# Kernel tuning notes

Measured on AMD Instinct MI355X. Metric: run time of the kernel, lower is better.

Reference implementation:

```python
import jax, jax.numpy as jnp
import numpy as np

SCALES = (16, 32, 64, 128)
P = 8
D = 1024
H = 16
DEPTH = 8
MLP = 4096
NCLS = 1000
PB = [(s // P) ** 2 for s in SCALES]            # [4, 16, 64, 256]
BLOCKS = [PB[0] + 1] + PB[1:]                    # [5, 16, 64, 256]
L = sum(BLOCKS)                                  # 341
PATCH_L = sum(PB)                                # 340
PD = P * P * 3                                   # 192
HD = D // H
EPS = 1e-6

# scale id per token (start token belongs to scale 0)
_SID = np.concatenate([np.full(n, k, dtype=np.int32) for k, n in enumerate(BLOCKS)])
# additive block-causal mask: token in scale q may attend to scales <= q
_ALLOW = _SID[None, :] <= _SID[:, None]
MASK = jnp.where(jnp.asarray(_ALLOW), 0.0, -1e30).astype(jnp.float32)  # [L, L]
SID = jnp.asarray(_SID)


def _ln(x):
    m = jnp.mean(x, axis=-1, keepdims=True)
    v = jnp.var(x, axis=-1, keepdims=True)
    return (x - m) / jnp.sqrt(v + EPS)


def _l2n(t):
    n = jnp.sqrt(jnp.sum(t * t, axis=-1, keepdims=True))
    return t / jnp.maximum(n, 1e-12)


def setup_inputs() -> dict:
    key = jax.random.key(0)
    ks = jax.random.split(key, 16)
    s = 0.02
    inp = {
        "patches": jax.random.normal(ks[0], (8, PATCH_L, PD), jnp.float32),
        "labels": jax.random.randint(ks[1], (8,), 0, NCLS),
        "W_patch": s * jax.random.normal(ks[2], (PD, D), jnp.float32),
        "b_patch": jnp.zeros((D,), jnp.float32),
        "pos": s * jax.random.normal(ks[3], (1, L, D), jnp.float32),
        "scale_emb": s * jax.random.normal(ks[4], (len(SCALES), D), jnp.float32),
        "class_emb": s * jax.random.normal(ks[5], (NCLS + 1, D), jnp.float32),
        "ada_W": s * jax.random.normal(ks[6], (DEPTH, D, 6 * D), jnp.float32),
        "ada_b": jnp.zeros((DEPTH, 6 * D), jnp.float32),
        "qkv_W": s * jax.random.normal(ks[7], (DEPTH, D, 3 * D), jnp.float32),
        "qkv_b": jnp.zeros((DEPTH, 3 * D), jnp.float32),
        "q_scale": jnp.zeros((DEPTH, 1, 1, H, 1), jnp.float32),  # log-scale per head
        "proj_W": s * jax.random.normal(ks[8], (DEPTH, D, D), jnp.float32),
        "proj_b": jnp.zeros((DEPTH, D), jnp.float32),
        "fc1_W": s * jax.random.normal(ks[9], (DEPTH, D, MLP), jnp.float32),
        "fc1_b": jnp.zeros((DEPTH, MLP), jnp.float32),
        "fc2_W": s * jax.random.normal(ks[10], (DEPTH, MLP, D), jnp.float32),
        "fc2_b": jnp.zeros((DEPTH, D), jnp.float32),
        "head_ada_W": s * jax.random.normal(ks[11], (D, 2 * D), jnp.float32),
        "head_ada_b": jnp.zeros((2 * D,), jnp.float32),
        "head_W": s * jax.random.normal(ks[12], (D, PD), jnp.float32),
        "head_b": jnp.zeros((PD,), jnp.float32),
    }
    return inp


def reference(patches, labels, W_patch, b_patch, pos, scale_emb, class_emb,
              ada_W, ada_b, qkv_W, qkv_b, q_scale, proj_W, proj_b,
              fc1_W, fc1_b, fc2_W, fc2_b, head_ada_W, head_ada_b, head_W, head_b):
    B = patches.shape[0]
    cond = class_emb[labels]                              # [B, D]
    tok = patches @ W_patch + b_patch                     # [B, PATCH_L, D]
    x = jnp.concatenate([cond[:, None, :], tok], axis=1)  # [B, L, D]
    x = x + pos + scale_emb[SID]

    for i in range(DEPTH):
        ada = jax.nn.silu(cond) @ ada_W[i] + ada_b[i]     # [B, 6D]
        g1, g2, s1, s2, sh1, sh2 = [a[:, None, :] for a in jnp.split(ada, 6, axis=-1)]
        # attention branch
        h = _ln(x) * (s1 + 1.0) + sh1
        qkv = (h @ qkv_W[i] + qkv_b[i]).reshape(B, L, 3, H, HD)
        q, k, v = qkv[:, :, 0], qkv[:, :, 1], qkv[:, :, 2]  # [B, L, H, HD]
        q = _l2n(q) * jnp.exp(q_scale[i])                  # attn_l2_norm
        k = _l2n(k)
        scores = jnp.einsum("bqhd,bkhd->bhqk", q, k) + MASK
        attn = jax.nn.softmax(scores, axis=-1)
        o = jnp.einsum("bhqk,bkhd->bqhd", attn, v).reshape(B, L, D)
        x = x + g1 * (o @ proj_W[i] + proj_b[i])
        # mlp branch
        h2 = _ln(x) * (s2 + 1.0) + sh2
        m = jax.nn.gelu(h2 @ fc1_W[i] + fc1_b[i]) @ fc2_W[i] + fc2_b[i]
        x = x + g2 * m

    ada = jax.nn.silu(cond) @ head_ada_W + head_ada_b     # [B, 2D]
    sc, sh = [a[:, None, :] for a in jnp.split(ada, 2, axis=-1)]
    x = _ln(x) * (sc + 1.0) + sh
    return x @ head_W + head_b                            # [B, L, PD]
```

## Files before the change

kernel.cpp:

```cpp
#include <hip/hip_runtime.h>

typedef unsigned short ushort_t;
typedef __bf16 bf16x8 __attribute__((ext_vector_type(8)));
typedef float f32x4 __attribute__((ext_vector_type(4)));

#define DEV __device__ __forceinline__

DEV ushort_t f2bf(float x) {
  union { float f; unsigned u; } v; v.f = x;
  unsigned r = v.u + 0x7FFFu + ((v.u >> 16) & 1u);
  return (ushort_t)(r >> 16);
}
DEV float bf2f(ushort_t h) {
  union { unsigned u; float f; } v; v.u = (unsigned)h << 16;
  return v.f;
}
DEV int sid_of(int l) { return l < 5 ? 0 : (l < 21 ? 1 : (l < 85 ? 2 : 3)); }
DEV float fast_tanh(float u) { return 1.0f - 2.0f / (__expf(2.0f * u) + 1.0f); }
DEV float gelu_f(float x) {
  float u = 0.7978845608028654f * (x + 0.044715f * x * x * x);
  return 0.5f * x * (1.0f + fast_tanh(u));
}
DEV float silu_f(float x) { return x / (1.0f + __expf(-x)); }
DEV f32x4 mfma16(bf16x8 a, bf16x8 b, f32x4 c) {
  return __builtin_amdgcn_mfma_f32_16x16x32_bf16(a, b, c, 0, 0, 0);
}

DEV void gload16(const void* src, void* dst) {
  __builtin_amdgcn_global_load_lds(
      (const __attribute__((address_space(1))) void*)(uintptr_t)src,
      (__attribute__((address_space(3))) void*)(uintptr_t)dst, 16, 0, 0);
}

__global__ __launch_bounds__(256) void k_cond_x0(
    const int* __restrict__ labels, const float* __restrict__ class_emb,
    const float* __restrict__ pos, const float* __restrict__ semb,
    float* __restrict__ cond, float* __restrict__ x) {
  int b = blockIdx.x, t = threadIdx.x;
  int lab = labels[b];
  float4 cv = *(const float4*)&class_emb[(size_t)lab * 1024 + t * 4];
  *(float4*)&cond[(size_t)b * 1024 + t * 4] = cv;
  float4 pv = *(const float4*)&pos[t * 4];
  float4 sv = *(const float4*)&semb[t * 4];
  float4 xv;
  xv.x = cv.x + pv.x + sv.x; xv.y = cv.y + pv.y + sv.y;
  xv.z = cv.z + pv.z + sv.z; xv.w = cv.w + pv.w + sv.w;
  *(float4*)&x[(size_t)b * 341 * 1024 + t * 4] = xv;
}

__global__ __launch_bounds__(256) void k_convert(const float* __restrict__ src,
                                                 ushort_t* __restrict__ dst, int n4) {
  int i = blockIdx.x * 256 + threadIdx.x;
  if (i < n4) {
    float4 v = *(const float4*)&src[(size_t)i * 4];
    uint2 pk;
    pk.x = (unsigned)f2bf(v.x) | ((unsigned)f2bf(v.y) << 16);
    pk.y = (unsigned)f2bf(v.z) | ((unsigned)f2bf(v.w) << 16);
    *(uint2*)&dst[(size_t)i * 4] = pk;
  }
}

__global__ __launch_bounds__(256) void k_transpose(const float* __restrict__ src,
                                                   ushort_t* __restrict__ dst, int K, int N) {
  __shared__ ushort_t tile[32][33];
  int z = blockIdx.z;
  src += (size_t)z * K * N;
  dst += (size_t)z * K * N;
  int k0 = blockIdx.y * 32, n0 = blockIdx.x * 32;
  int t = threadIdx.x;
  int r = t >> 3, c = (t & 7) * 4;
  float4 v = *(const float4*)&src[(size_t)(k0 + r) * N + n0 + c];
  tile[r][c] = f2bf(v.x); tile[r][c + 1] = f2bf(v.y);
  tile[r][c + 2] = f2bf(v.z); tile[r][c + 3] = f2bf(v.w);
  __syncthreads();
  ushort_t o0 = tile[c][r], o1 = tile[c + 1][r], o2 = tile[c + 2][r], o3 = tile[c + 3][r];
  uint2 pk;
  pk.x = (unsigned)o0 | ((unsigned)o1 << 16);
  pk.y = (unsigned)o2 | ((unsigned)o3 << 16);
  *(uint2*)&dst[(size_t)(n0 + r) * K + k0 + c] = pk;
}

__global__ __launch_bounds__(256) void k_ada(const float* __restrict__ cond,
    const float* __restrict__ ada_W, const float* __restrict__ ada_b,
    const float* __restrict__ hada_W, const float* __restrict__ hada_b,
    float* __restrict__ ada_out, float* __restrict__ hada_out) {
  int gy = blockIdx.y;
  bool head = (gy == 8);
  int Nw = head ? 2048 : 6144;
  int n0 = blockIdx.x * 64;
  if (n0 >= Nw) return;
  __shared__ float sc[8 * 1024];
  __shared__ float red[4][64][8];
  int t = threadIdx.x;
  for (int i = t; i < 2048; i += 256) {
    float4 cv = *(const float4*)&cond[(size_t)i * 4];
    float* d = &sc[i * 4];
    d[0] = silu_f(cv.x); d[1] = silu_f(cv.y); d[2] = silu_f(cv.z); d[3] = silu_f(cv.w);
  }
  __syncthreads();
  const float* W = head ? hada_W : ada_W + (size_t)gy * 1024 * 6144;
  const float* bs = head ? hada_b : ada_b + (size_t)gy * 6144;
  float* op = head ? hada_out : ada_out + (size_t)gy * 8 * 6144;
  int col = n0 + (t & 63), kq = t >> 6;
  float acc[8] = {0.f, 0.f, 0.f, 0.f, 0.f, 0.f, 0.f, 0.f};
  for (int k = kq * 256; k < kq * 256 + 256; ++k) {
    float wv = W[(size_t)k * Nw + col];
#pragma unroll
    for (int b2 = 0; b2 < 8; ++b2) acc[b2] += wv * sc[b2 * 1024 + k];
  }
#pragma unroll
  for (int b2 = 0; b2 < 8; ++b2) red[kq][t & 63][b2] = acc[b2];
  __syncthreads();
  if (t < 64) {
    int colc = n0 + t;
    float bias = bs[colc];
#pragma unroll
    for (int b2 = 0; b2 < 8; ++b2) {
      float v = red[0][t][b2] + red[1][t][b2] + red[2][t][b2] + red[3][t][b2] + bias;
      op[(size_t)b2 * Nw + colc] = v;
    }
  }
}

__global__ __launch_bounds__(256) void k_ln(const float* __restrict__ x,
    ushort_t* __restrict__ hout, const float* __restrict__ ada,
    int stride, int soff, int shoff) {
  int row = blockIdx.x, t = threadIdx.x;
  int b = row / 341;
  const float* xr = x + (size_t)row * 1024;
  float4 xv = *(const float4*)&xr[t * 4];
  float s = xv.x + xv.y + xv.z + xv.w;
  float ss = xv.x * xv.x + xv.y * xv.y + xv.z * xv.z + xv.w * xv.w;
#pragma unroll
  for (int off = 1; off < 64; off <<= 1) { s += __shfl_xor(s, off); ss += __shfl_xor(ss, off); }
  __shared__ float red[8];
  int w = t >> 6, lane = t & 63;
  if (lane == 0) { red[w] = s; red[w + 4] = ss; }
  __syncthreads();
  s = red[0] + red[1] + red[2] + red[3];
  ss = red[4] + red[5] + red[6] + red[7];
  float mean = s * (1.f / 1024.f);
  float var = ss * (1.f / 1024.f) - mean * mean;
  float rstd = rsqrtf(var + 1e-6f);
  const float* ar = ada + (size_t)b * stride;
  float xe[4] = {xv.x, xv.y, xv.z, xv.w};
  ushort_t tmp[4];
#pragma unroll
  for (int j = 0; j < 4; ++j) {
    int n = t * 4 + j;
    float val = (xe[j] - mean) * rstd * (1.f + ar[soff + n]) + ar[shoff + n];
    tmp[j] = f2bf(val);
  }
  uint2 pk;
  pk.x = (unsigned)tmp[0] | ((unsigned)tmp[1] << 16);
  pk.y = (unsigned)tmp[2] | ((unsigned)tmp[3] << 16);
  *(uint2*)&hout[(size_t)row * 1024 + t * 4] = pk;
}

template <int EPI, int BM>
__global__ __launch_bounds__(256, 3) void k_gemm(
    const ushort_t* __restrict__ A, const ushort_t* __restrict__ Bt,
    const float* __restrict__ bias, float* __restrict__ fout,
    ushort_t* __restrict__ bfout, const float* __restrict__ aux,
    float* __restrict__ xres, const float* __restrict__ pos,
    const float* __restrict__ semb, int M, int N, int K, int KS) {
  constexpr int NI = (BM == 128) ? 4 : 2;
  constexpr int WNB = (BM == 128) ? 64 : 32;
  __shared__ ushort_t aT[2][BM * 32];
  __shared__ ushort_t bT[2][128 * 32];
  int tid = threadIdx.x;
  int lane = tid & 63, w = tid >> 6;
  int WR = (BM == 128) ? (w >> 1) : 0;
  int WC = (BM == 128) ? (w & 1) : w;

  int gx = gridDim.x;
  int nwg = gx * gridDim.y;
  int orig = blockIdx.y * gx + blockIdx.x;
  int q = nwg >> 3, r8 = nwg & 7;
  int xcd = orig & 7, idx = orig >> 3;
  int lin = (xcd < r8 ? xcd * (q + 1) : r8 * (q + 1) + (xcd - r8) * q) + idx;
  int bx = lin % gx, by = lin / gx;

  int m0 = by * BM, n0 = bx * 128;
  int kbase = blockIdx.z * KS;
  f32x4 acc[4][NI];
#pragma unroll
  for (int i = 0; i < 4; ++i)
#pragma unroll
    for (int j = 0; j < NI; ++j) acc[i][j] = (f32x4){0.f, 0.f, 0.f, 0.f};

  int lrow = lane & 15;
  int csw = (lrow >> 1) & 3;
  int coff = ((lane >> 4) ^ csw) * 8;

  int s_row0 = tid >> 2, s_u = tid & 3;
  int s_c = s_u ^ ((s_row0 >> 1) & 3);
  int aR0 = m0 + s_row0; if (aR0 > M - 1) aR0 = M - 1;
  int bR0 = n0 + s_row0; if (bR0 > N - 1) bR0 = N - 1;
  int aR1 = m0 + s_row0 + 64; if (aR1 > M - 1) aR1 = M - 1;
  int bR1 = n0 + s_row0 + 64; if (bR1 > N - 1) bR1 = N - 1;
  const ushort_t* aSrc0 = A + (size_t)aR0 * K + kbase + s_c * 8;
  const ushort_t* aSrc1 = A + (size_t)aR1 * K + kbase + s_c * 8;
  const ushort_t* bSrc0 = Bt + (size_t)bR0 * K + kbase + s_c * 8;
  const ushort_t* bSrc1 = Bt + (size_t)bR1 * K + kbase + s_c * 8;
  int slot0 = w * 512, slot1 = 2048 + w * 512;

  int nsteps = KS >> 5;
  auto STAGE = [&](int k0, int buf) {
    gload16(aSrc0 + k0, &aT[buf][slot0]);
    if constexpr (BM == 128) gload16(aSrc1 + k0, &aT[buf][slot1]);
    gload16(bSrc0 + k0, &bT[buf][slot0]);
    gload16(bSrc1 + k0, &bT[buf][slot1]);
  };

  STAGE(0, 0);
  int cur = 0;
  for (int s = 0; s < nsteps; ++s) {
    int kn = (s + 1 < nsteps) ? ((s + 1) << 5) : 0;
    STAGE(kn, cur ^ 1);
    if constexpr (BM == 128)
      asm volatile("s_waitcnt vmcnt(4)" ::: "memory");
    else
      asm volatile("s_waitcnt vmcnt(3)" ::: "memory");
    __builtin_amdgcn_sched_barrier(0);
    __builtin_amdgcn_s_barrier();
    __builtin_amdgcn_sched_barrier(0);
    bf16x8 af[4], bb[NI];
#pragma unroll
    for (int mi = 0; mi < 4; ++mi)
      af[mi] = *(const bf16x8*)&aT[cur][(WR * 64 + mi * 16 + lrow) * 32 + coff];
#pragma unroll
    for (int ni = 0; ni < NI; ++ni)
      bb[ni] = *(const bf16x8*)&bT[cur][(WC * WNB + ni * 16 + lrow) * 32 + coff];
#pragma unroll
    for (int mi = 0; mi < 4; ++mi)
#pragma unroll
      for (int ni = 0; ni < NI; ++ni)
        acc[mi][ni] = mfma16(af[mi], bb[ni], acc[mi][ni]);
    __builtin_amdgcn_sched_barrier(0);
    __builtin_amdgcn_s_barrier();
    __builtin_amdgcn_sched_barrier(0);
    cur ^= 1;
  }

  if constexpr (EPI == 6) {
    int nb = n0 + WC * 64;
    int gh = nb >> 6;
    float qse = (gh < 16) ? __expf(aux[gh]) : 1.0f;
    bool dn = gh < 32;
#pragma unroll
    for (int mi = 0; mi < 4; ++mi) {
#pragma unroll
      for (int r = 0; r < 4; ++r) {
        float vv[4]; float ss = 0.f;
#pragma unroll
        for (int ni = 0; ni < 4; ++ni) {
          vv[ni] = acc[mi][ni][r] + bias[nb + ni * 16 + lrow];
          ss += vv[ni] * vv[ni];
        }
        if (dn) {
          ss += __shfl_xor(ss, 1); ss += __shfl_xor(ss, 2);
          ss += __shfl_xor(ss, 4); ss += __shfl_xor(ss, 8);
          float rn = qse / fmaxf(sqrtf(ss), 1e-12f);
#pragma unroll
          for (int ni = 0; ni < 4; ++ni) vv[ni] *= rn;
        }
        int gm = m0 + WR * 64 + mi * 16 + (lane >> 4) * 4 + r;
        if (gm < M) {
#pragma unroll
          for (int ni = 0; ni < 4; ++ni)
            bfout[(size_t)gm * N + nb + ni * 16 + lrow] = f2bf(vv[ni]);
        }
      }
    }
  } else {
#pragma unroll
    for (int mi = 0; mi < 4; ++mi) {
#pragma unroll
      for (int ni = 0; ni < NI; ++ni) {
#pragma unroll
        for (int r = 0; r < 4; ++r) {
          int gm = m0 + WR * 64 + mi * 16 + (lane >> 4) * 4 + r;
          int gn = n0 + WC * WNB + ni * 16 + lrow;
          if (gm >= M || gn >= N) continue;
          if constexpr (EPI == 7) {
            fout[(size_t)blockIdx.z * M * N + (size_t)gm * N + gn] = acc[mi][ni][r];
          } else {
            float v = acc[mi][ni][r] + bias[gn];
            if constexpr (EPI == 1) {
              int b = gm / 341;
              xres[(size_t)gm * 1024 + gn] += aux[(size_t)b * 6144 + gn] * v;
            } else if constexpr (EPI == 2) {
              bfout[(size_t)gm * N + gn] = f2bf(gelu_f(v));
            } else if constexpr (EPI == 4) {
              int b = gm / 340, l = gm % 340 + 1;
              float val = v + pos[(size_t)l * 1024 + gn] + semb[(size_t)sid_of(l) * 1024 + gn];
              xres[((size_t)(b * 341 + l)) * 1024 + gn] = val;
            }
          }
        }
      }
    }
  }
}

template <int MODE>
__global__ __launch_bounds__(256) void k_comb(const float* __restrict__ p,
    const float* __restrict__ bias, const float* __restrict__ aux,
    float* __restrict__ xres, float* __restrict__ out, int N, int nsplit) {
  int row = blockIdx.x, t = threadIdx.x;
  size_t stride = (size_t)2728 * N;
  if constexpr (MODE == 0) {
    int c = t * 4;
    float4 s = *(const float4*)&p[(size_t)row * N + c];
    for (int sp = 1; sp < nsplit; ++sp) {
      float4 qq = *(const float4*)&p[sp * stride + (size_t)row * N + c];
      s.x += qq.x; s.y += qq.y; s.z += qq.z; s.w += qq.w;
    }
    float4 bv = *(const float4*)&bias[c];
    int b = row / 341;
    const float* ar = aux + (size_t)b * 6144 + c;
    float4 xv = *(float4*)&xres[(size_t)row * 1024 + c];
    xv.x += ar[0] * (s.x + bv.x);
    xv.y += ar[1] * (s.y + bv.y);
    xv.z += ar[2] * (s.z + bv.z);
    xv.w += ar[3] * (s.w + bv.w);
    *(float4*)&xres[(size_t)row * 1024 + c] = xv;
  } else {
    if (t < 48) {
      int c = t * 4;
      float4 s = *(const float4*)&p[(size_t)row * N + c];
      for (int sp = 1; sp < nsplit; ++sp) {
        float4 qq = *(const float4*)&p[sp * stride + (size_t)row * N + c];
        s.x += qq.x; s.y += qq.y; s.z += qq.z; s.w += qq.w;
      }
      float4 bv = *(const float4*)&bias[c];
      s.x += bv.x; s.y += bv.y; s.z += bv.z; s.w += bv.w;
      *(float4*)&out[(size_t)row * N + c] = s;
    }
  }
}

__global__ __launch_bounds__(256) void k_attn(
    const ushort_t* __restrict__ qkv, ushort_t* __restrict__ o) {
  int qt = blockIdx.x, h = blockIdx.y, b = blockIdx.z;
  int t = threadIdx.x, lane = t & 63, w = t >> 6;
  int q0 = qt * 64;
  __shared__ ushort_t qT[64 * 72], kT[64 * 72], vS[64 * 72], vT[64 * 72];
  __shared__ ushort_t pT[4][16 * 72];
#pragma unroll
  for (int i = 0; i < 2; ++i) {
    int vid = t + 256 * i;
    int row = vid >> 3, seg = (vid & 7) * 8;
    int l = q0 + row; if (l > 340) l = 340;
    uint4 v = *(const uint4*)&qkv[((size_t)(b * 341 + l)) * 3072 + h * 64 + seg];
    *(uint4*)&qT[row * 72 + seg] = v;
  }
  int lrow = lane & 15, lk8 = (lane >> 4) * 8;
  int sq[4];
  float mrun[4], lsum[4];
  f32x4 accO[4];
#pragma unroll
  for (int r = 0; r < 4; ++r) {
    int lq = q0 + w * 16 + (lane >> 4) * 4 + r;
    sq[r] = sid_of(lq < 341 ? lq : 340);
    mrun[r] = -1e30f;
    lsum[r] = 0.f;
  }
#pragma unroll
  for (int d = 0; d < 4; ++d) accO[d] = (f32x4){0.f, 0.f, 0.f, 0.f};
  int sq_max = sid_of(q0 + 63 < 341 ? q0 + 63 : 340);
  int vd = t >> 2, vlseg = (t & 3) * 16;
  for (int c = 0; c < 6; ++c) {
    if (sid_of(c * 64) > sq_max) continue;
#pragma unroll
    for (int i = 0; i < 2; ++i) {
      int vid = t + 256 * i;
      int row = vid >> 3, seg = (vid & 7) * 8;
      int l = c * 64 + row; if (l > 340) l = 340;
      size_t base = ((size_t)(b * 341 + l)) * 3072 + h * 64 + seg;
      uint4 kv = *(const uint4*)&qkv[base + 1024];
      uint4 vv = *(const uint4*)&qkv[base + 2048];
      *(uint4*)&kT[row * 72 + seg] = kv;
      *(uint4*)&vS[row * 72 + seg] = vv;
    }
    __syncthreads();
    ushort_t tmp[16];
#pragma unroll
    for (int j = 0; j < 16; ++j) tmp[j] = vS[(vlseg + j) * 72 + vd];
    f32x4 sf[4];
#pragma unroll
    for (int nf = 0; nf < 4; ++nf) sf[nf] = (f32x4){0.f, 0.f, 0.f, 0.f};
    __builtin_amdgcn_s_setprio(1);
#pragma unroll
    for (int ks = 0; ks < 2; ++ks) {
      bf16x8 aq = *(const bf16x8*)&qT[(w * 16 + lrow) * 72 + ks * 32 + lk8];
#pragma unroll
      for (int nf = 0; nf < 4; ++nf) {
        bf16x8 bk = *(const bf16x8*)&kT[(nf * 16 + lrow) * 72 + ks * 32 + lk8];
        sf[nf] = mfma16(aq, bk, sf[nf]);
      }
    }
    __builtin_amdgcn_s_setprio(0);
#pragma unroll
    for (int nf = 0; nf < 4; ++nf) {
      int lk = c * 64 + nf * 16 + lrow;
      int sk = lk < 341 ? sid_of(lk) : 9;
#pragma unroll
      for (int r = 0; r < 4; ++r)
        if (sk > sq[r]) sf[nf][r] = -1e30f;
    }
    float rs[4];
#pragma unroll
    for (int r = 0; r < 4; ++r) {
      float m = sf[0][r];
      m = fmaxf(m, sf[1][r]); m = fmaxf(m, sf[2][r]); m = fmaxf(m, sf[3][r]);
#pragma unroll
      for (int off = 1; off < 16; off <<= 1) m = fmaxf(m, __shfl_xor(m, off));
      float mn = fmaxf(mrun[r], m);
      float scl = __expf(mrun[r] - mn);
      mrun[r] = mn;
      lsum[r] *= scl;
#pragma unroll
      for (int d = 0; d < 4; ++d) accO[d][r] *= scl;
      rs[r] = 0.f;
    }
    ushort_t* pw = &pT[w][0];
#pragma unroll
    for (int nf = 0; nf < 4; ++nf) {
#pragma unroll
      for (int r = 0; r < 4; ++r) {
        float p = __expf(sf[nf][r] - mrun[r]);
        rs[r] += p;
        pw[((lane >> 4) * 4 + r) * 72 + nf * 16 + lrow] = f2bf(p);
      }
    }
#pragma unroll
    for (int r = 0; r < 4; ++r) {
      float sum = rs[r];
#pragma unroll
      for (int off = 1; off < 16; off <<= 1) sum += __shfl_xor(sum, off);
      lsum[r] += sum;
    }
    {
      uint4 s0, s1;
      s0.x = (unsigned)tmp[0] | ((unsigned)tmp[1] << 16);
      s0.y = (unsigned)tmp[2] | ((unsigned)tmp[3] << 16);
      s0.z = (unsigned)tmp[4] | ((unsigned)tmp[5] << 16);
      s0.w = (unsigned)tmp[6] | ((unsigned)tmp[7] << 16);
      s1.x = (unsigned)tmp[8] | ((unsigned)tmp[9] << 16);
      s1.y = (unsigned)tmp[10] | ((unsigned)tmp[11] << 16);
      s1.z = (unsigned)tmp[12] | ((unsigned)tmp[13] << 16);
      s1.w = (unsigned)tmp[14] | ((unsigned)tmp[15] << 16);
      *(uint4*)&vT[vd * 72 + vlseg] = s0;
      *(uint4*)&vT[vd * 72 + vlseg + 8] = s1;
    }
    __syncthreads();
    __builtin_amdgcn_s_setprio(1);
#pragma unroll
    for (int ks = 0; ks < 2; ++ks) {
      bf16x8 ap = *(const bf16x8*)&pw[lrow * 72 + ks * 32 + lk8];
#pragma unroll
      for (int d = 0; d < 4; ++d) {
        bf16x8 bv = *(const bf16x8*)&vT[(d * 16 + lrow) * 72 + ks * 32 + lk8];
        accO[d] = mfma16(ap, bv, accO[d]);
      }
    }
    __builtin_amdgcn_s_setprio(0);
  }
#pragma unroll
  for (int d = 0; d < 4; ++d) {
#pragma unroll
    for (int r = 0; r < 4; ++r) {
      int lq = q0 + w * 16 + (lane >> 4) * 4 + r;
      if (lq < 341) {
        float ov = accO[d][r] / fmaxf(lsum[r], 1e-30f);
        o[((size_t)(b * 341 + lq)) * 1024 + h * 64 + d * 16 + lrow] = f2bf(ov);
      }
    }
  }
}

extern "C" void kernel_launch(void* const* d_in, const int* in_sizes, int n_in,
                              void* d_out, int out_size, void* d_ws, size_t ws_size,
                              hipStream_t stream) {
  const float* patches   = (const float*)d_in[0];
  const int*   labels    = (const int*)d_in[1];
  const float* W_patch   = (const float*)d_in[2];
  const float* b_patch   = (const float*)d_in[3];
  const float* pos       = (const float*)d_in[4];
  const float* scale_emb = (const float*)d_in[5];
  const float* class_emb = (const float*)d_in[6];
  const float* ada_W     = (const float*)d_in[7];
  const float* ada_b     = (const float*)d_in[8];
  const float* qkv_W     = (const float*)d_in[9];
  const float* qkv_b     = (const float*)d_in[10];
  const float* q_scale   = (const float*)d_in[11];
  const float* proj_W    = (const float*)d_in[12];
  const float* proj_b    = (const float*)d_in[13];
  const float* fc1_W     = (const float*)d_in[14];
  const float* fc1_b     = (const float*)d_in[15];
  const float* fc2_W     = (const float*)d_in[16];
  const float* fc2_b     = (const float*)d_in[17];
  const float* hada_W    = (const float*)d_in[18];
  const float* hada_b    = (const float*)d_in[19];
  const float* head_W    = (const float*)d_in[20];
  const float* head_b    = (const float*)d_in[21];
  (void)in_sizes; (void)n_in; (void)out_size; (void)ws_size;

  char* wsb = (char*)d_ws;
  size_t off = 0;
  auto alloc = [&](size_t bytes) -> void* {
    void* p = wsb + off;
    off = (off + bytes + 255) & ~(size_t)255;
    return p;
  };

  float*    f_cond   = (float*)alloc(8 * 1024 * 4);
  float*    f_ada    = (float*)alloc((size_t)8 * 8 * 6144 * 4);
  float*    f_hada   = (float*)alloc(8 * 2048 * 4);
  float*    f_x      = (float*)alloc((size_t)2728 * 1024 * 4);
  ushort_t* u_h      = (ushort_t*)alloc((size_t)2728 * 1024 * 2);
  ushort_t* u_qkv    = (ushort_t*)alloc((size_t)2728 * 3072 * 2);
  ushort_t* u_o      = (ushort_t*)alloc((size_t)2728 * 1024 * 2);
  ushort_t* u_mid    = (ushort_t*)alloc((size_t)2728 * 4096 * 2);
  float*    f_part   = (float*)alloc((size_t)2 * 2728 * 1024 * 4);
  ushort_t* u_patch  = (ushort_t*)alloc((size_t)2720 * 192 * 2);
  ushort_t* u_qkvt   = (ushort_t*)alloc((size_t)8 * 3072 * 1024 * 2);
  ushort_t* u_projt  = (ushort_t*)alloc((size_t)8 * 1024 * 1024 * 2);
  ushort_t* u_fc1t   = (ushort_t*)alloc((size_t)8 * 4096 * 1024 * 2);
  ushort_t* u_fc2t   = (ushort_t*)alloc((size_t)8 * 1024 * 4096 * 2);
  ushort_t* u_wpt    = (ushort_t*)alloc((size_t)1024 * 192 * 2);
  ushort_t* u_wht    = (ushort_t*)alloc((size_t)192 * 1024 * 2);

  const int MT = 22;
  const int MT64 = 43;

  k_cond_x0<<<8, 256, 0, stream>>>(labels, class_emb, pos, scale_emb, f_cond, f_x);
  k_transpose<<<dim3(32, 6, 1), 256, 0, stream>>>(W_patch, u_wpt, 192, 1024);
  k_transpose<<<dim3(6, 32, 1), 256, 0, stream>>>(head_W, u_wht, 1024, 192);
  k_convert<<<510, 256, 0, stream>>>(patches, u_patch, 130560);
  k_ada<<<dim3(96, 9), 256, 0, stream>>>(f_cond, ada_W, ada_b, hada_W, hada_b, f_ada, f_hada);
  k_transpose<<<dim3(96, 32, 8), 256, 0, stream>>>(qkv_W, u_qkvt, 1024, 3072);
  k_transpose<<<dim3(32, 32, 8), 256, 0, stream>>>(proj_W, u_projt, 1024, 1024);
  k_transpose<<<dim3(128, 32, 8), 256, 0, stream>>>(fc1_W, u_fc1t, 1024, 4096);
  k_transpose<<<dim3(32, 128, 8), 256, 0, stream>>>(fc2_W, u_fc2t, 4096, 1024);

  k_gemm<4, 128><<<dim3(8, MT), 256, 0, stream>>>(u_patch, u_wpt, b_patch, nullptr, nullptr,
                                                  nullptr, f_x, pos, scale_emb, 2720, 1024, 192, 192);

  for (int i = 0; i < 8; ++i) {
    const float* adaL = f_ada + (size_t)i * 8 * 6144;
    k_ln<<<2728, 256, 0, stream>>>(f_x, u_h, adaL, 6144, 2048, 4096);
    k_gemm<6, 128><<<dim3(24, MT), 256, 0, stream>>>(u_h, u_qkvt + (size_t)i * 3072 * 1024,
                                                     qkv_b + (size_t)i * 3072, nullptr, u_qkv,
                                                     q_scale + (size_t)i * 16, nullptr, nullptr,
                                                     nullptr, 2728, 3072, 1024, 1024);
    k_attn<<<dim3(6, 16, 8), 256, 0, stream>>>(u_qkv, u_o);
    k_gemm<1, 64><<<dim3(8, MT64), 256, 0, stream>>>(u_o, u_projt + (size_t)i * 1024 * 1024,
                                                     proj_b + (size_t)i * 1024, nullptr,
                                                     nullptr, adaL, f_x, nullptr, nullptr,
                                                     2728, 1024, 1024, 1024);
    k_ln<<<2728, 256, 0, stream>>>(f_x, u_h, adaL, 6144, 3072, 5120);
    k_gemm<2, 128><<<dim3(32, MT), 256, 0, stream>>>(u_h, u_fc1t + (size_t)i * 4096 * 1024,
                                                     fc1_b + (size_t)i * 4096, nullptr,
                                                     u_mid, nullptr, nullptr, nullptr, nullptr,
                                                     2728, 4096, 1024, 1024);
    k_gemm<7, 64><<<dim3(8, MT64, 2), 256, 0, stream>>>(u_mid, u_fc2t + (size_t)i * 4096 * 1024,
                                                        nullptr, f_part,
                                                        nullptr, nullptr, nullptr, nullptr, nullptr,
                                                        2728, 1024, 4096, 2048);
    k_comb<0><<<2728, 256, 0, stream>>>(f_part, fc2_b + (size_t)i * 1024, adaL + 1024,
                                        f_x, nullptr, 1024, 2);
  }

  k_ln<<<2728, 256, 0, stream>>>(f_x, u_h, f_hada, 2048, 0, 1024);
  k_gemm<7, 64><<<dim3(2, MT64, 4), 256, 0, stream>>>(u_h, u_wht, nullptr, f_part, nullptr,
                                                      nullptr, nullptr, nullptr, nullptr,
                                                      2728, 192, 1024, 256);
  k_comb<1><<<2728, 256, 0, stream>>>(f_part, head_b, nullptr, nullptr, (float*)d_out, 192, 4);
}
```

Measured before the change: 1.809 ms.

## Fuse residual combine with LayerNorm, triple-buffer GEMM, prefetch attention KV

Adds a k_comb_ln kernel that applies the gated residual update (from split-K partials plus bias) and then computes the next adaLN-modulated LayerNorm in the same pass. This removes the separate k_ln launches and one extra read of x per sublayer. The proj GEMM now writes raw partials instead of doing the residual in its epilogue. The GEMM moves from double to triple LDS buffering with deeper vmcnt waits, and attention register-prefetches the next K/V chunk and uses a fixed chunk count. The larger LDS footprint may reduce occupancy, and the proj output now takes an extra fp32 round trip through memory.

```diff
diff --git a/kernel.cpp b/kernel.cpp
--- a/kernel.cpp
+++ b/kernel.cpp
@@ -10,10 +10,6 @@
   union { float f; unsigned u; } v; v.f = x;
   unsigned r = v.u + 0x7FFFu + ((v.u >> 16) & 1u);
   return (ushort_t)(r >> 16);
-}
-DEV float bf2f(ushort_t h) {
-  union { unsigned u; float f; } v; v.u = (unsigned)h << 16;
-  return v.f;
 }
 DEV int sid_of(int l) { return l < 5 ? 0 : (l < 21 ? 1 : (l < 85 ? 2 : 3)); }
 DEV float fast_tanh(float u) { return 1.0f - 2.0f / (__expf(2.0f * u) + 1.0f); }
@@ -25,7 +21,6 @@
 DEV f32x4 mfma16(bf16x8 a, bf16x8 b, f32x4 c) {
   return __builtin_amdgcn_mfma_f32_16x16x32_bf16(a, b, c, 0, 0, 0);
 }
-
 DEV void gload16(const void* src, void* dst) {
   __builtin_amdgcn_global_load_lds(
       (const __attribute__((address_space(1))) void*)(uintptr_t)src,
@@ -157,6 +152,56 @@
   *(uint2*)&hout[(size_t)row * 1024 + t * 4] = pk;
 }
 
+__global__ __launch_bounds__(256) void k_comb_ln(
+    const float* __restrict__ p, const float* __restrict__ bias,
+    const float* __restrict__ adag, int goff,
+    float* __restrict__ x, const float* __restrict__ adaln,
+    int lnstride, int soff, int shoff,
+    ushort_t* __restrict__ hout, int nsplit) {
+  int row = blockIdx.x, t = threadIdx.x;
+  int b = row / 341;
+  int c = t * 4;
+  float4 s4 = *(const float4*)&p[(size_t)row * 1024 + c];
+  if (nsplit == 2) {
+    float4 q2 = *(const float4*)&p[(size_t)2728 * 1024 + (size_t)row * 1024 + c];
+    s4.x += q2.x; s4.y += q2.y; s4.z += q2.z; s4.w += q2.w;
+  }
+  float4 bv = *(const float4*)&bias[c];
+  const float* gr = adag + (size_t)b * 6144 + goff + c;
+  float4 xv = *(float4*)&x[(size_t)row * 1024 + c];
+  xv.x += gr[0] * (s4.x + bv.x);
+  xv.y += gr[1] * (s4.y + bv.y);
+  xv.z += gr[2] * (s4.z + bv.z);
+  xv.w += gr[3] * (s4.w + bv.w);
+  *(float4*)&x[(size_t)row * 1024 + c] = xv;
+  float sm = xv.x + xv.y + xv.z + xv.w;
+  float ss = xv.x * xv.x + xv.y * xv.y + xv.z * xv.z + xv.w * xv.w;
+#pragma unroll
+  for (int off = 1; off < 64; off <<= 1) { sm += __shfl_xor(sm, off); ss += __shfl_xor(ss, off); }
+  __shared__ float red[8];
+  int w = t >> 6, lane = t & 63;
+  if (lane == 0) { red[w] = sm; red[w + 4] = ss; }
+  __syncthreads();
+  sm = red[0] + red[1] + red[2] + red[3];
+  ss = red[4] + red[5] + red[6] + red[7];
+  float mean = sm * (1.f / 1024.f);
+  float var = ss * (1.f / 1024.f) - mean * mean;
+  float rstd = rsqrtf(var + 1e-6f);
+  const float* ar = adaln + (size_t)b * lnstride;
+  float xe[4] = {xv.x, xv.y, xv.z, xv.w};
+  ushort_t tmp[4];
+#pragma unroll
+  for (int j = 0; j < 4; ++j) {
+    int n = c + j;
+    float val = (xe[j] - mean) * rstd * (1.f + ar[soff + n]) + ar[shoff + n];
+    tmp[j] = f2bf(val);
+  }
+  uint2 pk;
+  pk.x = (unsigned)tmp[0] | ((unsigned)tmp[1] << 16);
+  pk.y = (unsigned)tmp[2] | ((unsigned)tmp[3] << 16);
+  *(uint2*)&hout[(size_t)row * 1024 + c] = pk;
+}
+
 template <int EPI, int BM>
 __global__ __launch_bounds__(256, 3) void k_gemm(
     const ushort_t* __restrict__ A, const ushort_t* __restrict__ Bt,
@@ -166,8 +211,8 @@
     const float* __restrict__ semb, int M, int N, int K, int KS) {
   constexpr int NI = (BM == 128) ? 4 : 2;
   constexpr int WNB = (BM == 128) ? 64 : 32;
-  __shared__ ushort_t aT[2][BM * 32];
-  __shared__ ushort_t bT[2][128 * 32];
+  __shared__ ushort_t aT[3][BM * 32];
+  __shared__ ushort_t bT[3][128 * 32];
   int tid = threadIdx.x;
   int lane = tid & 63, w = tid >> 6;
   int WR = (BM == 128) ? (w >> 1) : 0;
@@ -214,24 +259,26 @@
   };
 
   STAGE(0, 0);
-  int cur = 0;
+  STAGE(32, 1);
+  int ibuf = 0;
   for (int s = 0; s < nsteps; ++s) {
-    int kn = (s + 1 < nsteps) ? ((s + 1) << 5) : 0;
-    STAGE(kn, cur ^ 1);
+    int st = ibuf + 2; if (st >= 3) st -= 3;
+    int kn = (s + 2 < nsteps) ? ((s + 2) << 5) : 0;
+    STAGE(kn, st);
     if constexpr (BM == 128)
-      asm volatile("s_waitcnt vmcnt(4)" ::: "memory");
+      asm volatile("s_waitcnt vmcnt(8)" ::: "memory");
     else
-      asm volatile("s_waitcnt vmcnt(3)" ::: "memory");
+      asm volatile("s_waitcnt vmcnt(6)" ::: "memory");
     __builtin_amdgcn_sched_barrier(0);
     __builtin_amdgcn_s_barrier();
     __builtin_amdgcn_sched_barrier(0);
     bf16x8 af[4], bb[NI];
 #pragma unroll
     for (int mi = 0; mi < 4; ++mi)
-      af[mi] = *(const bf16x8*)&aT[cur][(WR * 64 + mi * 16 + lrow) * 32 + coff];
+      af[mi] = *(const bf16x8*)&aT[ibuf][(WR * 64 + mi * 16 + lrow) * 32 + coff];
 #pragma unroll
     for (int ni = 0; ni < NI; ++ni)
-      bb[ni] = *(const bf16x8*)&bT[cur][(WC * WNB + ni * 16 + lrow) * 32 + coff];
+      bb[ni] = *(const bf16x8*)&bT[ibuf][(WC * WNB + ni * 16 + lrow) * 32 + coff];
 #pragma unroll
     for (int mi = 0; mi < 4; ++mi)
 #pragma unroll
@@ -240,7 +287,7 @@
     __builtin_amdgcn_sched_barrier(0);
     __builtin_amdgcn_s_barrier();
     __builtin_amdgcn_sched_barrier(0);
-    cur ^= 1;
+    ibuf = (ibuf + 1 == 3) ? 0 : ibuf + 1;
   }
 
   if constexpr (EPI == 6) {
@@ -287,10 +334,7 @@
             fout[(size_t)blockIdx.z * M * N + (size_t)gm * N + gn] = acc[mi][ni][r];
           } else {
             float v = acc[mi][ni][r] + bias[gn];
-            if constexpr (EPI == 1) {
-              int b = gm / 341;
-              xres[(size_t)gm * 1024 + gn] += aux[(size_t)b * 6144 + gn] * v;
-            } else if constexpr (EPI == 2) {
+            if constexpr (EPI == 2) {
               bfout[(size_t)gm * N + gn] = f2bf(gelu_f(v));
             } else if constexpr (EPI == 4) {
               int b = gm / 340, l = gm % 340 + 1;
@@ -304,13 +348,12 @@
   }
 }
 
-template <int MODE>
-__global__ __launch_bounds__(256) void k_comb(const float* __restrict__ p,
-    const float* __restrict__ bias, const float* __restrict__ aux,
-    float* __restrict__ xres, float* __restrict__ out, int N, int nsplit) {
+__global__ __launch_bounds__(256) void k_comb_head(const float* __restrict__ p,
+    const float* __restrict__ bias, float* __restrict__ out, int nsplit) {
   int row = blockIdx.x, t = threadIdx.x;
+  const int N = 192;
   size_t stride = (size_t)2728 * N;
-  if constexpr (MODE == 0) {
+  if (t < 48) {
     int c = t * 4;
     float4 s = *(const float4*)&p[(size_t)row * N + c];
     for (int sp = 1; sp < nsplit; ++sp) {
@@ -318,26 +361,8 @@
       s.x += qq.x; s.y += qq.y; s.z += qq.z; s.w += qq.w;
     }
     float4 bv = *(const float4*)&bias[c];
-    int b = row / 341;
-    const float* ar = aux + (size_t)b * 6144 + c;
-    float4 xv = *(float4*)&xres[(size_t)row * 1024 + c];
-    xv.x += ar[0] * (s.x + bv.x);
-    xv.y += ar[1] * (s.y + bv.y);
-    xv.z += ar[2] * (s.z + bv.z);
-    xv.w += ar[3] * (s.w + bv.w);
-    *(float4*)&xres[(size_t)row * 1024 + c] = xv;
-  } else {
-    if (t < 48) {
-      int c = t * 4;
-      float4 s = *(const float4*)&p[(size_t)row * N + c];
-      for (int sp = 1; sp < nsplit; ++sp) {
-        float4 qq = *(const float4*)&p[sp * stride + (size_t)row * N + c];
-        s.x += qq.x; s.y += qq.y; s.z += qq.z; s.w += qq.w;
-      }
-      float4 bv = *(const float4*)&bias[c];
-      s.x += bv.x; s.y += bv.y; s.z += bv.z; s.w += bv.w;
-      *(float4*)&out[(size_t)row * N + c] = s;
-    }
+    s.x += bv.x; s.y += bv.y; s.z += bv.z; s.w += bv.w;
+    *(float4*)&out[(size_t)row * N + c] = s;
   }
 }
 
@@ -369,22 +394,33 @@
   }
 #pragma unroll
   for (int d = 0; d < 4; ++d) accO[d] = (f32x4){0.f, 0.f, 0.f, 0.f};
-  int sq_max = sid_of(q0 + 63 < 341 ? q0 + 63 : 340);
+  int nch = (qt == 0) ? 2 : 6;
   int vd = t >> 2, vlseg = (t & 3) * 16;
-  for (int c = 0; c < 6; ++c) {
-    if (sid_of(c * 64) > sq_max) continue;
+
+  uint4 kr[2], vr[2];
+  auto ldkv = [&](int c) {
 #pragma unroll
     for (int i = 0; i < 2; ++i) {
       int vid = t + 256 * i;
       int row = vid >> 3, seg = (vid & 7) * 8;
       int l = c * 64 + row; if (l > 340) l = 340;
       size_t base = ((size_t)(b * 341 + l)) * 3072 + h * 64 + seg;
-      uint4 kv = *(const uint4*)&qkv[base + 1024];
-      uint4 vv = *(const uint4*)&qkv[base + 2048];
-      *(uint4*)&kT[row * 72 + seg] = kv;
-      *(uint4*)&vS[row * 72 + seg] = vv;
-    }
+      kr[i] = *(const uint4*)&qkv[base + 1024];
+      vr[i] = *(const uint4*)&qkv[base + 2048];
+    }
+  };
+  ldkv(0);
+  for (int c = 0; c < nch; ++c) {
     __syncthreads();
+#pragma unroll
+    for (int i = 0; i < 2; ++i) {
+      int vid = t + 256 * i;
+      int row = vid >> 3, seg = (vid & 7) * 8;
+      *(uint4*)&kT[row * 72 + seg] = kr[i];
+      *(uint4*)&vS[row * 72 + seg] = vr[i];
+    }
+    __syncthreads();
+    if (c + 1 < nch) ldkv(c + 1);
     ushort_t tmp[16];
 #pragma unroll
     for (int j = 0; j < 16; ++j) tmp[j] = vS[(vlseg + j) * 72 + vd];
@@ -548,35 +584,41 @@
 
   k_gemm<4, 128><<<dim3(8, MT), 256, 0, stream>>>(u_patch, u_wpt, b_patch, nullptr, nullptr,
                                                   nullptr, f_x, pos, scale_emb, 2720, 1024, 192, 192);
+  k_ln<<<2728, 256, 0, stream>>>(f_x, u_h, f_ada, 6144, 2048, 4096);
 
   for (int i = 0; i < 8; ++i) {
     const float* adaL = f_ada + (size_t)i * 8 * 6144;
-    k_ln<<<2728, 256, 0, stream>>>(f_x, u_h, adaL, 6144, 2048, 4096);
     k_gemm<6, 128><<<dim3(24, MT), 256, 0, stream>>>(u_h, u_qkvt + (size_t)i * 3072 * 1024,
                                                      qkv_b + (size_t)i * 3072, nullptr, u_qkv,
                                                      q_scale + (size_t)i * 16, nullptr, nullptr,
                                                      nullptr, 2728, 3072, 1024, 1024);
     k_attn<<<dim3(6, 16, 8), 256, 0, stream>>>(u_qkv, u_o);
-    k_gemm<1, 64><<<dim3(8, MT64), 256, 0, stream>>>(u_o, u_projt + (size_t)i * 1024 * 1024,
-                                                     proj_b + (size_t)i * 1024, nullptr,
-                                                     nullptr, adaL, f_x, nullptr, nullptr,
-                                                     2728, 1024, 1024, 1024);
-    k_ln<<<2728, 256, 0, stream>>>(f_x, u_h, adaL, 6144, 3072, 5120);
+    k_gemm<7, 64><<<dim3(8, MT64, 1), 256, 0, stream>>>(u_o, u_projt + (size_t)i * 1024 * 1024,
+                                                        nullptr, f_part, nullptr, nullptr,
+                                                        nullptr, nullptr, nullptr,
+                                                        2728, 1024, 1024, 1024);
+    k_comb_ln<<<2728, 256, 0, stream>>>(f_part, proj_b + (size_t)i * 1024, adaL, 0,
+                                        f_x, adaL, 6144, 3072, 5120, u_h, 1);
     k_gemm<2, 128><<<dim3(32, MT), 256, 0, stream>>>(u_h, u_fc1t + (size_t)i * 4096 * 1024,
                                                      fc1_b + (size_t)i * 4096, nullptr,
                                                      u_mid, nullptr, nullptr, nullptr, nullptr,
                                                      2728, 4096, 1024, 1024);
     k_gemm<7, 64><<<dim3(8, MT64, 2), 256, 0, stream>>>(u_mid, u_fc2t + (size_t)i * 4096 * 1024,
-                                                        nullptr, f_part,
-                                                        nullptr, nullptr, nullptr, nullptr, nullptr,
+                                                        nullptr, f_part, nullptr, nullptr,
+                                                        nullptr, nullptr, nullptr,
                                                         2728, 1024, 4096, 2048);
-    k_comb<0><<<2728, 256, 0, stream>>>(f_part, fc2_b + (size_t)i * 1024, adaL + 1024,
-                                        f_x, nullptr, 1024, 2);
-  }
-
-  k_ln<<<2728, 256, 0, stream>>>(f_x, u_h, f_hada, 2048, 0, 1024);
+    if (i < 7) {
+      k_comb_ln<<<2728, 256, 0, stream>>>(f_part, fc2_b + (size_t)i * 1024, adaL, 1024,
+                                          f_x, f_ada + (size_t)(i + 1) * 8 * 6144,
+                                          6144, 2048, 4096, u_h, 2);
+    } else {
+      k_comb_ln<<<2728, 256, 0, stream>>>(f_part, fc2_b + (size_t)i * 1024, adaL, 1024,
+                                          f_x, f_hada, 2048, 0, 1024, u_h, 2);
+    }
+  }
+
   k_gemm<7, 64><<<dim3(2, MT64, 4), 256, 0, stream>>>(u_h, u_wht, nullptr, f_part, nullptr,
                                                       nullptr, nullptr, nullptr, nullptr,
                                                       2728, 192, 1024, 256);
-  k_comb<1><<<2728, 256, 0, stream>>>(f_part, head_b, nullptr, nullptr, (float*)d_out, 192, 4);
-}
+  k_comb_head<<<2728, 256, 0, stream>>>(f_part, head_b, (float*)d_out, 4);
+}
```

New measurement: 1.999 ms. +10.5%, slower.
